# Kernel tuning notes

Measured on AMD Instinct MI355X. Metric: run time of the kernel, lower is better.

The kernel has to match this reference:

```python
import jax, jax.numpy as jnp
import numpy as np

ATT = 256  # att_fc_size
MIN_W = 32  # min_width_feat
EPS = 1e-5  # InstanceNorm eps


def setup_inputs() -> dict:
    key = jax.random.key(0)
    ks = jax.random.split(key, 16)
    B, C, H, W = 32, 256, 128, 256
    hid = 256
    s = 0.02
    inp = {
        'features': jax.random.normal(ks[0], (B, C, H, W), jnp.float32),
        'prev_attn_weights': jax.random.uniform(ks[1], (B, H), jnp.float32),
        'coverage_vector': jax.random.uniform(ks[2], (B, H), jnp.float32) * 2.0,
        'hidden_h': jax.random.normal(ks[3], (1, B, hid), jnp.float32),
        # dense_width: Linear(min_width, 1)
        'w_width': jax.random.normal(ks[4], (MIN_W, 1), jnp.float32) * s,
        'b_width': jnp.zeros((1,), jnp.float32),
        # dense_enc: Linear(C, att)
        'w_enc': jax.random.normal(ks[5], (C, ATT), jnp.float32) * s,
        'b_enc': jnp.zeros((ATT,), jnp.float32),
        # conv_block: Conv1d(2, 16, k=15, pad=7)  (OIW layout)
        'conv_w': jax.random.normal(ks[6], (16, 2, 15), jnp.float32) * s,
        'conv_b': jnp.zeros((16,), jnp.float32),
        # dense_conv_block: Linear(16, att)
        'w_cb': jax.random.normal(ks[7], (16, ATT), jnp.float32) * s,
        'b_cb': jnp.zeros((ATT,), jnp.float32),
        # dense_hidden: Linear(hidden, att)
        'w_hid': jax.random.normal(ks[8], (hid, ATT), jnp.float32) * s,
        'b_hid': jnp.zeros((ATT,), jnp.float32),
        # dense_align: Linear(att, 1)
        'w_align': jax.random.normal(ks[9], (ATT, 1), jnp.float32) * s,
        'b_align': jnp.zeros((1,), jnp.float32),
    }
    return inp


def reference(features, prev_attn_weights, coverage_vector, hidden_h,
              w_width, b_width, w_enc, b_enc, conv_w, conv_b,
              w_cb, b_cb, w_hid, b_hid, w_align, b_align):
    B, C, H, W = features.shape
    # AdaptiveMaxPool2d((None, MIN_W)) with W % MIN_W == 0 -> uniform window max
    hf = features.reshape(B, C, H, MIN_W, W // MIN_W).max(axis=-1)  # (B,C,H,MIN_W)
    # dense_width -> (B,C,H)
    h_features = (jnp.einsum('bchm,mo->bcho', hf, w_width) + b_width)[..., 0]
    # branch 1: dense_enc on (B,H,C)
    s = jnp.einsum('bhc,ca->bha', h_features.transpose(0, 2, 1), w_enc) + b_enc
    # location + coverage channels: (B,2,H)
    cat = jnp.stack([prev_attn_weights, jnp.clip(coverage_vector, 0.0, 1.0)], axis=1)
    # InstanceNorm1d (no affine): per (b, channel) over H
    mu = cat.mean(axis=-1, keepdims=True)
    var = cat.var(axis=-1, keepdims=True)
    cat = (cat - mu) * jax.lax.rsqrt(var + EPS)
    # Conv1d(2 -> 16, k=15, pad=7)
    conv = jax.lax.conv_general_dilated(
        cat, conv_w, window_strides=(1,), padding=[(7, 7)],
        dimension_numbers=('NCH', 'OIH', 'NCH')) + conv_b[None, :, None]  # (B,16,H)
    s = s + jnp.einsum('bhk,ka->bha', conv.transpose(0, 2, 1), w_cb) + b_cb
    # hidden branch: (1,B,hid) -> (1,B,att) -> (B,1,att), broadcasts over H
    hsum = (jnp.einsum('lbd,da->lba', hidden_h, w_hid) + b_hid).transpose(1, 0, 2)
    s = s + hsum
    s = jnp.tanh(s)
    align_score = jnp.einsum('bha,ao->bho', s, w_align) + b_align  # (B,H,1)
    attn = jax.nn.softmax(align_score, axis=1)  # softmax over H
    # context: features^T(H<->W) @ attn -> (B,C,W)
    context = jnp.einsum('bchw,bh->bcw', features, attn[..., 0])
    return context, attn[..., 0]
```

## Files before the change

### kernel.cpp

```cpp
#include <hip/hip_runtime.h>
#include <hip/hip_bf16.h>

#define B_DIM 32
#define C_DIM 256
#define H_DIM 128
#define W_DIM 256
#define ATT_DIM 256

__global__ __launch_bounds__(256) void ka_fused(
    const float* __restrict__ feat, const float* __restrict__ w_width,
    const float* __restrict__ b_width,
    const float* __restrict__ prev, const float* __restrict__ cov,
    const float* __restrict__ conv_w, const float* __restrict__ conv_b,
    const float* __restrict__ hidden, const float* __restrict__ w_hid,
    const float* __restrict__ b_hid, const float* __restrict__ b_enc,
    const float* __restrict__ b_cb,
    float* __restrict__ hf, float* __restrict__ convT, float* __restrict__ hsum)
{
  const int tid = threadIdx.x;
  const int bid = blockIdx.x;

  if (bid < 8192) {
    __shared__ float res[H_DIM];
    const int lane = tid & 63, w = tid >> 6;
    const int half = lane >> 5;
    const int m = lane & 31;
    const float wv = w_width[m];
    const float bw = b_width[0];
    const float* base = feat + (size_t)bid * H_DIM * W_DIM + m * 8;
#pragma unroll 4
    for (int i = 0; i < 16; i++) {
      const int h = w * 32 + i * 2 + half;
      const float4* p = reinterpret_cast<const float4*>(base + (size_t)h * W_DIM);
      float4 a = p[0], b2 = p[1];
      float mx = fmaxf(fmaxf(fmaxf(a.x, a.y), fmaxf(a.z, a.w)),
                       fmaxf(fmaxf(b2.x, b2.y), fmaxf(b2.z, b2.w)));
      float contrib = mx * wv;
#pragma unroll
      for (int off = 1; off <= 16; off <<= 1) contrib += __shfl_xor(contrib, off);
      if (m == 0) res[h] = contrib + bw;
    }
    __syncthreads();
    if (tid < H_DIM)
      hf[(size_t)bid * H_DIM + tid] = res[tid];
  } else if (bid < 8224) {
    const int b = bid - 8192;
    __shared__ float n0[H_DIM], n1[H_DIM];
    __shared__ float ws4[2][4];
    __shared__ float cw[480];
    for (int i = tid; i < 480; i += 256) cw[i] = conv_w[i];
    const int lane = tid & 63, wv2 = tid >> 6;
    float x0 = 0.f, x1 = 0.f;
    if (tid < 128) {
      x0 = prev[b * H_DIM + tid];
      x1 = cov[b * H_DIM + tid];
      x1 = fminf(fmaxf(x1, 0.0f), 1.0f);
      float s0 = x0, q0 = x0 * x0, s1 = x1, q1 = x1 * x1;
#pragma unroll
      for (int off = 32; off >= 1; off >>= 1) {
        s0 += __shfl_xor(s0, off); q0 += __shfl_xor(q0, off);
        s1 += __shfl_xor(s1, off); q1 += __shfl_xor(q1, off);
      }
      if (lane == 0) { ws4[wv2][0] = s0; ws4[wv2][1] = q0; ws4[wv2][2] = s1; ws4[wv2][3] = q1; }
    }
    __syncthreads();
    if (tid < 128) {
      float S0 = ws4[0][0] + ws4[1][0], Q0 = ws4[0][1] + ws4[1][1];
      float S1 = ws4[0][2] + ws4[1][2], Q1 = ws4[0][3] + ws4[1][3];
      const float rH = 1.0f / H_DIM;
      float mu0 = S0 * rH, mu1 = S1 * rH;
      float inv0 = 1.0f / sqrtf(Q0 * rH - mu0 * mu0 + 1e-5f);
      float inv1 = 1.0f / sqrtf(Q1 * rH - mu1 * mu1 + 1e-5f);
      n0[tid] = (x0 - mu0) * inv0;
      n1[tid] = (x1 - mu1) * inv1;
    }
    __syncthreads();
    if (tid < 128) {
      float o[16];
#pragma unroll
      for (int k = 0; k < 16; k++) o[k] = conv_b[k];
#pragma unroll
      for (int j = 0; j < 15; j++) {
        int hh = tid - 7 + j;
        if (hh >= 0 && hh < H_DIM) {
          float f0 = n0[hh], f1 = n1[hh];
#pragma unroll
          for (int k = 0; k < 16; k++)
            o[k] += f0 * cw[k * 30 + j] + f1 * cw[k * 30 + 15 + j];
        }
      }
      float* outp = convT + ((size_t)(b * H_DIM + tid)) * 16;
#pragma unroll
      for (int k = 0; k < 16; k++) outp[k] = o[k];
    }
  } else {
    const int b = bid - 8224;
    const int a = tid;
    float acc = b_hid[a] + b_enc[a] + b_cb[a];
    const float* hb = hidden + b * 256;
#pragma unroll 4
    for (int d = 0; d < 256; d++) acc += hb[d] * w_hid[d * ATT_DIM + a];
    hsum[b * ATT_DIM + a] = acc;
  }
}

__global__ __launch_bounds__(256) void kb_gemm_align(
    const float* __restrict__ hf, const float* __restrict__ convT,
    const float* __restrict__ hsum, const float* __restrict__ w_enc,
    const float* __restrict__ w_cb, const float* __restrict__ w_align,
    const float* __restrict__ b_align, float* __restrict__ align_out)
{
  __shared__ float At[C_DIM][12];
  __shared__ float Ct[16][9];
  __shared__ float red[8][ATT_DIM];
  const int tid = threadIdx.x;
  const int m0 = blockIdx.x * 8;
  const int b = m0 >> 7;
  const int h0 = m0 & 127;
  const float* hp = hf + ((size_t)(b * C_DIM + tid)) * H_DIM + h0;
  float4 r0 = *reinterpret_cast<const float4*>(hp);
  float4 r1 = *reinterpret_cast<const float4*>(hp + 4);
  *reinterpret_cast<float4*>(&At[tid][0]) = r0;
  *reinterpret_cast<float4*>(&At[tid][4]) = r1;
  if (tid < 128) {
    int m = tid >> 4, k = tid & 15;
    Ct[k][m] = convT[(size_t)(b * H_DIM + h0) * 16 + tid];
  }
  __syncthreads();
  float acc[8];
#pragma unroll
  for (int m = 0; m < 8; m++) acc[m] = 0.0f;
  const float* wep = w_enc + tid;
#pragma unroll 4
  for (int k = 0; k < C_DIM; k++) {
    float bv = wep[k * ATT_DIM];
    const float4 a0 = *reinterpret_cast<const float4*>(&At[k][0]);
    const float4 a1 = *reinterpret_cast<const float4*>(&At[k][4]);
    acc[0] += a0.x * bv; acc[1] += a0.y * bv; acc[2] += a0.z * bv; acc[3] += a0.w * bv;
    acc[4] += a1.x * bv; acc[5] += a1.y * bv; acc[6] += a1.z * bv; acc[7] += a1.w * bv;
  }
#pragma unroll
  for (int k = 0; k < 16; k++) {
    float bv = w_cb[k * ATT_DIM + tid];
#pragma unroll
    for (int m = 0; m < 8; m++) acc[m] += Ct[k][m] * bv;
  }
  const float hs = hsum[b * ATT_DIM + tid];
  const float wa = w_align[tid];
#pragma unroll
  for (int m = 0; m < 8; m++)
    red[m][tid] = tanhf(acc[m] + hs) * wa;
  __syncthreads();
  const int lane = tid & 63, wid = tid >> 6;
  const float ba = b_align[0];
  for (int m = wid; m < 8; m += 4) {
    float s = red[m][lane] + red[m][lane + 64] + red[m][lane + 128] + red[m][lane + 192];
#pragma unroll
    for (int off = 32; off >= 1; off >>= 1) s += __shfl_xor(s, off);
    if (lane == 0) align_out[m0 + m] = s + ba;
  }
}

__global__ __launch_bounds__(256) void kc_context(
    const float* __restrict__ feat, const float* __restrict__ align,
    float* __restrict__ attn_out, float* __restrict__ ctx)
{
  const int bc = 8191 - blockIdx.x;
  const int b = bc >> 8, c = bc & 255;
  const int tid = threadIdx.x;
  __shared__ float al[H_DIM], at[H_DIM];
  if (tid < H_DIM) al[tid] = align[(b << 7) + tid];
  __syncthreads();
  if (tid < 64) {
    float a0 = al[tid], a1 = al[tid + 64];
    float mx = fmaxf(a0, a1);
#pragma unroll
    for (int off = 32; off >= 1; off >>= 1) mx = fmaxf(mx, __shfl_xor(mx, off));
    float e0 = expf(a0 - mx), e1 = expf(a1 - mx);
    float s = e0 + e1;
#pragma unroll
    for (int off = 32; off >= 1; off >>= 1) s += __shfl_xor(s, off);
    float inv = 1.0f / s;
    at[tid] = e0 * inv;
    at[tid + 64] = e1 * inv;
  }
  __syncthreads();
  if (c == 0 && tid < H_DIM) attn_out[(b << 7) + tid] = at[tid];
  const int g = tid >> 6, lane = tid & 63;
  const float* base = feat + (size_t)bc * H_DIM * W_DIM + lane * 4;
  float4 acc0 = make_float4(0.f, 0.f, 0.f, 0.f);
  float4 acc1 = make_float4(0.f, 0.f, 0.f, 0.f);
#pragma unroll 2
  for (int h = g; h < H_DIM; h += 8) {
    float4 v0 = *reinterpret_cast<const float4*>(base + (size_t)h * W_DIM);
    float4 v1 = *reinterpret_cast<const float4*>(base + (size_t)(h + 4) * W_DIM);
    float a0 = at[h], a1 = at[h + 4];
    acc0.x += v0.x * a0; acc0.y += v0.y * a0; acc0.z += v0.z * a0; acc0.w += v0.w * a0;
    acc1.x += v1.x * a1; acc1.y += v1.y * a1; acc1.z += v1.z * a1; acc1.w += v1.w * a1;
  }
  __shared__ float4 part[4][64];
  float4 acc;
  acc.x = acc0.x + acc1.x; acc.y = acc0.y + acc1.y;
  acc.z = acc0.z + acc1.z; acc.w = acc0.w + acc1.w;
  part[g][lane] = acc;
  __syncthreads();
  if (tid < 64) {
    float4 r0 = part[0][tid], r1 = part[1][tid], r2 = part[2][tid], r3 = part[3][tid];
    float4 o;
    o.x = r0.x + r1.x + r2.x + r3.x;
    o.y = r0.y + r1.y + r2.y + r3.y;
    o.z = r0.z + r1.z + r2.z + r3.z;
    o.w = r0.w + r1.w + r2.w + r3.w;
    *reinterpret_cast<float4*>(ctx + (size_t)bc * W_DIM + tid * 4) = o;
  }
}

extern "C" void kernel_launch(void* const* d_in, const int* in_sizes, int n_in,
                              void* d_out, int out_size, void* d_ws, size_t ws_size,
                              hipStream_t stream)
{
  const float* feat    = (const float*)d_in[0];
  const float* prev    = (const float*)d_in[1];
  const float* cov     = (const float*)d_in[2];
  const float* hidden  = (const float*)d_in[3];
  const float* w_width = (const float*)d_in[4];
  const float* b_width = (const float*)d_in[5];
  const float* w_enc   = (const float*)d_in[6];
  const float* b_enc   = (const float*)d_in[7];
  const float* conv_w  = (const float*)d_in[8];
  const float* conv_b  = (const float*)d_in[9];
  const float* w_cb    = (const float*)d_in[10];
  const float* b_cb    = (const float*)d_in[11];
  const float* w_hid   = (const float*)d_in[12];
  const float* b_hid   = (const float*)d_in[13];
  const float* w_align = (const float*)d_in[14];
  const float* b_align = (const float*)d_in[15];

  float* ctx_out  = (float*)d_out;
  float* attn_out = (float*)d_out + (size_t)B_DIM * C_DIM * W_DIM;

  float* ws    = (float*)d_ws;
  float* hf    = ws;
  float* convT = hf + 1048576;
  float* hsum  = convT + 65536;
  float* align = hsum + 8192;

  ka_fused<<<dim3(8192 + 32 + 32), dim3(256), 0, stream>>>(
      feat, w_width, b_width, prev, cov, conv_w, conv_b,
      hidden, w_hid, b_hid, b_enc, b_cb, hf, convT, hsum);
  kb_gemm_align<<<dim3((B_DIM * H_DIM) / 8), dim3(256), 0, stream>>>(
      hf, convT, hsum, w_enc, w_cb, w_align, b_align, align);
  kc_context<<<dim3(B_DIM * C_DIM), dim3(256), 0, stream>>>(
      feat, align, attn_out, ctx_out);
}
```

Before: 400.6 us.

## Fuse three kernels into one flag-synchronized persistent pipeline per batch

Merges the pooling, GEMM/align and context kernels into a single launch. Blocks are grouped per batch (256 pool, 16 gemm, 256 context) and synchronized through global atomic counters with spin-waits, so later batches' stages can overlap earlier batches' work and the kernel-boundary drains go away. It relies on block dispatch order to avoid deadlock and adds a memset and spin-wait overhead. The context stage also no longer runs in reverse order, so it may lose L2 reuse of recently read features.

```diff
diff --git a/kernel.cpp b/kernel.cpp
--- a/kernel.cpp
+++ b/kernel.cpp
@@ -1,55 +1,42 @@
 #include <hip/hip_runtime.h>
-#include <hip/hip_bf16.h>
 
 #define B_DIM 32
 #define C_DIM 256
 #define H_DIM 128
 #define W_DIM 256
 #define ATT_DIM 256
-
-__global__ __launch_bounds__(256) void ka_fused(
+#define GRP 528
+
+union Smem {
+  struct { float res[H_DIM]; } a;
+  struct { float n0[H_DIM], n1[H_DIM], ws4[2][4], cw[480]; } nc;
+  struct { float At[C_DIM][12]; float Ct[16][9]; float red[8][ATT_DIM]; } b;
+  struct { float al[H_DIM], at[H_DIM]; float4 part[4][64]; } c;
+};
+
+__global__ __launch_bounds__(256) void mega_pipeline(
     const float* __restrict__ feat, const float* __restrict__ w_width,
     const float* __restrict__ b_width,
     const float* __restrict__ prev, const float* __restrict__ cov,
     const float* __restrict__ conv_w, const float* __restrict__ conv_b,
     const float* __restrict__ hidden, const float* __restrict__ w_hid,
     const float* __restrict__ b_hid, const float* __restrict__ b_enc,
-    const float* __restrict__ b_cb,
-    float* __restrict__ hf, float* __restrict__ convT, float* __restrict__ hsum)
+    const float* __restrict__ b_cb, const float* __restrict__ w_enc,
+    const float* __restrict__ w_cb, const float* __restrict__ w_align,
+    const float* __restrict__ b_align,
+    float* __restrict__ hf, float* __restrict__ convT,
+    float* __restrict__ hsum, float* __restrict__ align_buf,
+    int* __restrict__ flags,
+    float* __restrict__ attn_out, float* __restrict__ ctx)
 {
+  __shared__ Smem sm;
   const int tid = threadIdx.x;
   const int bid = blockIdx.x;
 
-  if (bid < 8192) {
-    __shared__ float res[H_DIM];
-    const int lane = tid & 63, w = tid >> 6;
-    const int half = lane >> 5;
-    const int m = lane & 31;
-    const float wv = w_width[m];
-    const float bw = b_width[0];
-    const float* base = feat + (size_t)bid * H_DIM * W_DIM + m * 8;
-#pragma unroll 4
-    for (int i = 0; i < 16; i++) {
-      const int h = w * 32 + i * 2 + half;
-      const float4* p = reinterpret_cast<const float4*>(base + (size_t)h * W_DIM);
-      float4 a = p[0], b2 = p[1];
-      float mx = fmaxf(fmaxf(fmaxf(a.x, a.y), fmaxf(a.z, a.w)),
-                       fmaxf(fmaxf(b2.x, b2.y), fmaxf(b2.z, b2.w)));
-      float contrib = mx * wv;
-#pragma unroll
-      for (int off = 1; off <= 16; off <<= 1) contrib += __shfl_xor(contrib, off);
-      if (m == 0) res[h] = contrib + bw;
-    }
-    __syncthreads();
-    if (tid < H_DIM)
-      hf[(size_t)bid * H_DIM + tid] = res[tid];
-  } else if (bid < 8224) {
-    const int b = bid - 8192;
-    __shared__ float n0[H_DIM], n1[H_DIM];
-    __shared__ float ws4[2][4];
-    __shared__ float cw[480];
-    for (int i = tid; i < 480; i += 256) cw[i] = conv_w[i];
-    const int lane = tid & 63, wv2 = tid >> 6;
+  if (bid < B_DIM) {
+    const int b = bid;
+    for (int i = tid; i < 480; i += 256) sm.nc.cw[i] = conv_w[i];
+    const int wv2 = tid >> 6;
     float x0 = 0.f, x1 = 0.f;
     if (tid < 128) {
       x0 = prev[b * H_DIM + tid];
@@ -61,18 +48,21 @@
         s0 += __shfl_xor(s0, off); q0 += __shfl_xor(q0, off);
         s1 += __shfl_xor(s1, off); q1 += __shfl_xor(q1, off);
       }
-      if (lane == 0) { ws4[wv2][0] = s0; ws4[wv2][1] = q0; ws4[wv2][2] = s1; ws4[wv2][3] = q1; }
+      if ((tid & 63) == 0) {
+        sm.nc.ws4[wv2][0] = s0; sm.nc.ws4[wv2][1] = q0;
+        sm.nc.ws4[wv2][2] = s1; sm.nc.ws4[wv2][3] = q1;
+      }
     }
     __syncthreads();
     if (tid < 128) {
-      float S0 = ws4[0][0] + ws4[1][0], Q0 = ws4[0][1] + ws4[1][1];
-      float S1 = ws4[0][2] + ws4[1][2], Q1 = ws4[0][3] + ws4[1][3];
+      float S0 = sm.nc.ws4[0][0] + sm.nc.ws4[1][0], Q0 = sm.nc.ws4[0][1] + sm.nc.ws4[1][1];
+      float S1 = sm.nc.ws4[0][2] + sm.nc.ws4[1][2], Q1 = sm.nc.ws4[0][3] + sm.nc.ws4[1][3];
       const float rH = 1.0f / H_DIM;
       float mu0 = S0 * rH, mu1 = S1 * rH;
       float inv0 = 1.0f / sqrtf(Q0 * rH - mu0 * mu0 + 1e-5f);
       float inv1 = 1.0f / sqrtf(Q1 * rH - mu1 * mu1 + 1e-5f);
-      n0[tid] = (x0 - mu0) * inv0;
-      n1[tid] = (x1 - mu1) * inv1;
+      sm.nc.n0[tid] = (x0 - mu0) * inv0;
+      sm.nc.n1[tid] = (x1 - mu1) * inv1;
     }
     __syncthreads();
     if (tid < 128) {
@@ -83,135 +73,171 @@
       for (int j = 0; j < 15; j++) {
         int hh = tid - 7 + j;
         if (hh >= 0 && hh < H_DIM) {
-          float f0 = n0[hh], f1 = n1[hh];
+          float f0 = sm.nc.n0[hh], f1 = sm.nc.n1[hh];
 #pragma unroll
           for (int k = 0; k < 16; k++)
-            o[k] += f0 * cw[k * 30 + j] + f1 * cw[k * 30 + 15 + j];
+            o[k] += f0 * sm.nc.cw[k * 30 + j] + f1 * sm.nc.cw[k * 30 + 15 + j];
         }
       }
       float* outp = convT + ((size_t)(b * H_DIM + tid)) * 16;
 #pragma unroll
       for (int k = 0; k < 16; k++) outp[k] = o[k];
     }
-  } else {
-    const int b = bid - 8224;
+    __syncthreads();
+    if (tid == 0)
+      __hip_atomic_fetch_add(&flags[64], 1, __ATOMIC_RELEASE, __HIP_MEMORY_SCOPE_AGENT);
+  } else if (bid < 2 * B_DIM) {
+    const int b = bid - B_DIM;
     const int a = tid;
     float acc = b_hid[a] + b_enc[a] + b_cb[a];
     const float* hb = hidden + b * 256;
 #pragma unroll 4
     for (int d = 0; d < 256; d++) acc += hb[d] * w_hid[d * ATT_DIM + a];
     hsum[b * ATT_DIM + a] = acc;
-  }
-}
-
-__global__ __launch_bounds__(256) void kb_gemm_align(
-    const float* __restrict__ hf, const float* __restrict__ convT,
-    const float* __restrict__ hsum, const float* __restrict__ w_enc,
-    const float* __restrict__ w_cb, const float* __restrict__ w_align,
-    const float* __restrict__ b_align, float* __restrict__ align_out)
-{
-  __shared__ float At[C_DIM][12];
-  __shared__ float Ct[16][9];
-  __shared__ float red[8][ATT_DIM];
-  const int tid = threadIdx.x;
-  const int m0 = blockIdx.x * 8;
-  const int b = m0 >> 7;
-  const int h0 = m0 & 127;
-  const float* hp = hf + ((size_t)(b * C_DIM + tid)) * H_DIM + h0;
-  float4 r0 = *reinterpret_cast<const float4*>(hp);
-  float4 r1 = *reinterpret_cast<const float4*>(hp + 4);
-  *reinterpret_cast<float4*>(&At[tid][0]) = r0;
-  *reinterpret_cast<float4*>(&At[tid][4]) = r1;
-  if (tid < 128) {
-    int m = tid >> 4, k = tid & 15;
-    Ct[k][m] = convT[(size_t)(b * H_DIM + h0) * 16 + tid];
-  }
-  __syncthreads();
-  float acc[8];
-#pragma unroll
-  for (int m = 0; m < 8; m++) acc[m] = 0.0f;
-  const float* wep = w_enc + tid;
+    __syncthreads();
+    if (tid == 0)
+      __hip_atomic_fetch_add(&flags[64], 1, __ATOMIC_RELEASE, __HIP_MEMORY_SCOPE_AGENT);
+  } else {
+    const int e = bid - 2 * B_DIM;
+    const int b = e / GRP;
+    const int r = e - b * GRP;
+
+    if (r < 256) {
+      const int bc = b * C_DIM + r;
+      const int lane = tid & 63, w = tid >> 6;
+      const int half = lane >> 5;
+      const int m = lane & 31;
+      const float wv = w_width[m];
+      const float bw = b_width[0];
+      const float* base = feat + (size_t)bc * (H_DIM * W_DIM) + m * 8;
 #pragma unroll 4
-  for (int k = 0; k < C_DIM; k++) {
-    float bv = wep[k * ATT_DIM];
-    const float4 a0 = *reinterpret_cast<const float4*>(&At[k][0]);
-    const float4 a1 = *reinterpret_cast<const float4*>(&At[k][4]);
-    acc[0] += a0.x * bv; acc[1] += a0.y * bv; acc[2] += a0.z * bv; acc[3] += a0.w * bv;
-    acc[4] += a1.x * bv; acc[5] += a1.y * bv; acc[6] += a1.z * bv; acc[7] += a1.w * bv;
-  }
-#pragma unroll
-  for (int k = 0; k < 16; k++) {
-    float bv = w_cb[k * ATT_DIM + tid];
-#pragma unroll
-    for (int m = 0; m < 8; m++) acc[m] += Ct[k][m] * bv;
-  }
-  const float hs = hsum[b * ATT_DIM + tid];
-  const float wa = w_align[tid];
-#pragma unroll
-  for (int m = 0; m < 8; m++)
-    red[m][tid] = tanhf(acc[m] + hs) * wa;
-  __syncthreads();
-  const int lane = tid & 63, wid = tid >> 6;
-  const float ba = b_align[0];
-  for (int m = wid; m < 8; m += 4) {
-    float s = red[m][lane] + red[m][lane + 64] + red[m][lane + 128] + red[m][lane + 192];
-#pragma unroll
-    for (int off = 32; off >= 1; off >>= 1) s += __shfl_xor(s, off);
-    if (lane == 0) align_out[m0 + m] = s + ba;
-  }
-}
-
-__global__ __launch_bounds__(256) void kc_context(
-    const float* __restrict__ feat, const float* __restrict__ align,
-    float* __restrict__ attn_out, float* __restrict__ ctx)
-{
-  const int bc = 8191 - blockIdx.x;
-  const int b = bc >> 8, c = bc & 255;
-  const int tid = threadIdx.x;
-  __shared__ float al[H_DIM], at[H_DIM];
-  if (tid < H_DIM) al[tid] = align[(b << 7) + tid];
-  __syncthreads();
-  if (tid < 64) {
-    float a0 = al[tid], a1 = al[tid + 64];
-    float mx = fmaxf(a0, a1);
-#pragma unroll
-    for (int off = 32; off >= 1; off >>= 1) mx = fmaxf(mx, __shfl_xor(mx, off));
-    float e0 = expf(a0 - mx), e1 = expf(a1 - mx);
-    float s = e0 + e1;
-#pragma unroll
-    for (int off = 32; off >= 1; off >>= 1) s += __shfl_xor(s, off);
-    float inv = 1.0f / s;
-    at[tid] = e0 * inv;
-    at[tid + 64] = e1 * inv;
-  }
-  __syncthreads();
-  if (c == 0 && tid < H_DIM) attn_out[(b << 7) + tid] = at[tid];
-  const int g = tid >> 6, lane = tid & 63;
-  const float* base = feat + (size_t)bc * H_DIM * W_DIM + lane * 4;
-  float4 acc0 = make_float4(0.f, 0.f, 0.f, 0.f);
-  float4 acc1 = make_float4(0.f, 0.f, 0.f, 0.f);
+      for (int i = 0; i < 16; i++) {
+        const int h = w * 32 + i * 2 + half;
+        const float4* p = reinterpret_cast<const float4*>(base + (size_t)h * W_DIM);
+        float4 a4 = p[0], b4 = p[1];
+        float mx = fmaxf(fmaxf(fmaxf(a4.x, a4.y), fmaxf(a4.z, a4.w)),
+                         fmaxf(fmaxf(b4.x, b4.y), fmaxf(b4.z, b4.w)));
+        float contrib = mx * wv;
+#pragma unroll
+        for (int off = 1; off <= 16; off <<= 1) contrib += __shfl_xor(contrib, off);
+        if (m == 0) sm.a.res[h] = contrib + bw;
+      }
+      __syncthreads();
+      if (tid < H_DIM) hf[(size_t)bc * H_DIM + tid] = sm.a.res[tid];
+      __syncthreads();
+      if (tid == 0)
+        __hip_atomic_fetch_add(&flags[b], 1, __ATOMIC_RELEASE, __HIP_MEMORY_SCOPE_AGENT);
+    } else if (r < 272) {
+      if (tid == 0) {
+        while (__hip_atomic_load(&flags[b], __ATOMIC_RELAXED, __HIP_MEMORY_SCOPE_AGENT) < 256)
+          __builtin_amdgcn_s_sleep(8);
+        while (__hip_atomic_load(&flags[64], __ATOMIC_RELAXED, __HIP_MEMORY_SCOPE_AGENT) < 64)
+          __builtin_amdgcn_s_sleep(8);
+        __threadfence();
+      }
+      __syncthreads();
+      const int h0 = (r - 256) * 8;
+      const int m0 = b * H_DIM + h0;
+      const float* hp = hf + ((size_t)(b * C_DIM + tid)) * H_DIM + h0;
+      float4 r0 = *reinterpret_cast<const float4*>(hp);
+      float4 r1 = *reinterpret_cast<const float4*>(hp + 4);
+      *reinterpret_cast<float4*>(&sm.b.At[tid][0]) = r0;
+      *reinterpret_cast<float4*>(&sm.b.At[tid][4]) = r1;
+      if (tid < 128) {
+        int mm = tid >> 4, k = tid & 15;
+        sm.b.Ct[k][mm] = convT[(size_t)(b * H_DIM + h0) * 16 + tid];
+      }
+      __syncthreads();
+      float acc[8];
+#pragma unroll
+      for (int mm = 0; mm < 8; mm++) acc[mm] = 0.0f;
+      const float* wep = w_enc + tid;
+#pragma unroll 4
+      for (int k = 0; k < C_DIM; k++) {
+        float bv = wep[k * ATT_DIM];
+        const float4 a0 = *reinterpret_cast<const float4*>(&sm.b.At[k][0]);
+        const float4 a1 = *reinterpret_cast<const float4*>(&sm.b.At[k][4]);
+        acc[0] += a0.x * bv; acc[1] += a0.y * bv; acc[2] += a0.z * bv; acc[3] += a0.w * bv;
+        acc[4] += a1.x * bv; acc[5] += a1.y * bv; acc[6] += a1.z * bv; acc[7] += a1.w * bv;
+      }
+#pragma unroll
+      for (int k = 0; k < 16; k++) {
+        float bv = w_cb[k * ATT_DIM + tid];
+#pragma unroll
+        for (int mm = 0; mm < 8; mm++) acc[mm] += sm.b.Ct[k][mm] * bv;
+      }
+      const float hs = hsum[b * ATT_DIM + tid];
+      const float wa = w_align[tid];
+#pragma unroll
+      for (int mm = 0; mm < 8; mm++)
+        sm.b.red[mm][tid] = tanhf(acc[mm] + hs) * wa;
+      __syncthreads();
+      const int lane = tid & 63, wid = tid >> 6;
+      const float ba = b_align[0];
+      for (int mm = wid; mm < 8; mm += 4) {
+        float s = sm.b.red[mm][lane] + sm.b.red[mm][lane + 64] +
+                  sm.b.red[mm][lane + 128] + sm.b.red[mm][lane + 192];
+#pragma unroll
+        for (int off = 32; off >= 1; off >>= 1) s += __shfl_xor(s, off);
+        if (lane == 0) align_buf[m0 + mm] = s + ba;
+      }
+      __syncthreads();
+      if (tid == 0)
+        __hip_atomic_fetch_add(&flags[32 + b], 1, __ATOMIC_RELEASE, __HIP_MEMORY_SCOPE_AGENT);
+    } else {
+      if (tid == 0) {
+        while (__hip_atomic_load(&flags[32 + b], __ATOMIC_RELAXED, __HIP_MEMORY_SCOPE_AGENT) < 16)
+          __builtin_amdgcn_s_sleep(8);
+        __threadfence();
+      }
+      __syncthreads();
+      const int c = r - 272;
+      const int bc = b * C_DIM + c;
+      if (tid < H_DIM) sm.c.al[tid] = align_buf[(b << 7) + tid];
+      __syncthreads();
+      if (tid < 64) {
+        float a0 = sm.c.al[tid], a1 = sm.c.al[tid + 64];
+        float mx = fmaxf(a0, a1);
+#pragma unroll
+        for (int off = 32; off >= 1; off >>= 1) mx = fmaxf(mx, __shfl_xor(mx, off));
+        float e0 = expf(a0 - mx), e1 = expf(a1 - mx);
+        float s = e0 + e1;
+#pragma unroll
+        for (int off = 32; off >= 1; off >>= 1) s += __shfl_xor(s, off);
+        float inv = 1.0f / s;
+        sm.c.at[tid] = e0 * inv;
+        sm.c.at[tid + 64] = e1 * inv;
+      }
+      __syncthreads();
+      if (c == 0 && tid < H_DIM) attn_out[(b << 7) + tid] = sm.c.at[tid];
+      const int g = tid >> 6, lane = tid & 63;
+      const float* base = feat + (size_t)bc * (H_DIM * W_DIM) + lane * 4;
+      float4 acc0 = make_float4(0.f, 0.f, 0.f, 0.f);
+      float4 acc1 = make_float4(0.f, 0.f, 0.f, 0.f);
 #pragma unroll 2
-  for (int h = g; h < H_DIM; h += 8) {
-    float4 v0 = *reinterpret_cast<const float4*>(base + (size_t)h * W_DIM);
-    float4 v1 = *reinterpret_cast<const float4*>(base + (size_t)(h + 4) * W_DIM);
-    float a0 = at[h], a1 = at[h + 4];
-    acc0.x += v0.x * a0; acc0.y += v0.y * a0; acc0.z += v0.z * a0; acc0.w += v0.w * a0;
-    acc1.x += v1.x * a1; acc1.y += v1.y * a1; acc1.z += v1.z * a1; acc1.w += v1.w * a1;
-  }
-  __shared__ float4 part[4][64];
-  float4 acc;
-  acc.x = acc0.x + acc1.x; acc.y = acc0.y + acc1.y;
-  acc.z = acc0.z + acc1.z; acc.w = acc0.w + acc1.w;
-  part[g][lane] = acc;
-  __syncthreads();
-  if (tid < 64) {
-    float4 r0 = part[0][tid], r1 = part[1][tid], r2 = part[2][tid], r3 = part[3][tid];
-    float4 o;
-    o.x = r0.x + r1.x + r2.x + r3.x;
-    o.y = r0.y + r1.y + r2.y + r3.y;
-    o.z = r0.z + r1.z + r2.z + r3.z;
-    o.w = r0.w + r1.w + r2.w + r3.w;
-    *reinterpret_cast<float4*>(ctx + (size_t)bc * W_DIM + tid * 4) = o;
+      for (int h = g; h < H_DIM; h += 8) {
+        float4 v0 = *reinterpret_cast<const float4*>(base + (size_t)h * W_DIM);
+        float4 v1 = *reinterpret_cast<const float4*>(base + (size_t)(h + 4) * W_DIM);
+        float a0 = sm.c.at[h], a1 = sm.c.at[h + 4];
+        acc0.x += v0.x * a0; acc0.y += v0.y * a0; acc0.z += v0.z * a0; acc0.w += v0.w * a0;
+        acc1.x += v1.x * a1; acc1.y += v1.y * a1; acc1.z += v1.z * a1; acc1.w += v1.w * a1;
+      }
+      float4 acc;
+      acc.x = acc0.x + acc1.x; acc.y = acc0.y + acc1.y;
+      acc.z = acc0.z + acc1.z; acc.w = acc0.w + acc1.w;
+      sm.c.part[g][lane] = acc;
+      __syncthreads();
+      if (tid < 64) {
+        float4 p0 = sm.c.part[0][tid], p1 = sm.c.part[1][tid];
+        float4 p2 = sm.c.part[2][tid], p3 = sm.c.part[3][tid];
+        float4 o;
+        o.x = p0.x + p1.x + p2.x + p3.x;
+        o.y = p0.y + p1.y + p2.y + p3.y;
+        o.z = p0.z + p1.z + p2.z + p3.z;
+        o.w = p0.w + p1.w + p2.w + p3.w;
+        *reinterpret_cast<float4*>(ctx + (size_t)bc * W_DIM + tid * 4) = o;
+      }
+    }
   }
 }
 
@@ -239,17 +265,16 @@
   float* ctx_out  = (float*)d_out;
   float* attn_out = (float*)d_out + (size_t)B_DIM * C_DIM * W_DIM;
 
-  float* ws    = (float*)d_ws;
-  float* hf    = ws;
-  float* convT = hf + 1048576;
-  float* hsum  = convT + 65536;
-  float* align = hsum + 8192;
-
-  ka_fused<<<dim3(8192 + 32 + 32), dim3(256), 0, stream>>>(
+  float* ws       = (float*)d_ws;
+  float* hf       = ws;
+  float* convT    = hf + 1048576;
+  float* hsum     = convT + 65536;
+  float* align_b  = hsum + 8192;
+  int*   flags    = (int*)(align_b + 4096);
+
+  hipMemsetAsync(flags, 0, 512, stream);
+  mega_pipeline<<<dim3(2 * B_DIM + B_DIM * GRP), dim3(256), 0, stream>>>(
       feat, w_width, b_width, prev, cov, conv_w, conv_b,
-      hidden, w_hid, b_hid, b_enc, b_cb, hf, convT, hsum);
-  kb_gemm_align<<<dim3((B_DIM * H_DIM) / 8), dim3(256), 0, stream>>>(
-      hf, convT, hsum, w_enc, w_cb, w_align, b_align, align);
-  kc_context<<<dim3(B_DIM * C_DIM), dim3(256), 0, stream>>>(
-      feat, align, attn_out, ctx_out);
+      hidden, w_hid, b_hid, b_enc, b_cb, w_enc, w_cb, w_align, b_align,
+      hf, convT, hsum, align_b, flags, attn_out, ctx_out);
 }
```

After: 1.230 ms. 3.07x slower.
